# Performance work log

Measured on AMD Instinct MI355X. Metric: run time of the kernel, lower is better.

## Reference

```python
import jax, jax.numpy as jnp
import numpy as np

PAD_IDX = 0  # y_vocab.token_to_idx('<PAD>'); source also hard-codes argmax==0 as stop
B, N, M, V, T = 8, 6, 64, 32000, 8  # N = max_span, T = template_len


def setup_inputs() -> dict:
    key = jax.random.key(0)
    k1, k2, k3 = jax.random.split(key, 3)
    input_decodings = jax.random.normal(k1, (B, N, M, V), dtype=jnp.float32)
    template = jax.random.uniform(k2, (B, T, N + 1), dtype=jnp.float32)
    spans = jax.random.randint(k3, (B,), 0, N)
    return {"input_decodings": input_decodings, "template": template, "spans": spans}


def reference(input_decodings, template, spans):
    Bq, Nq, Mq, Vq = input_decodings.shape
    Tq = template.shape[1]
    # original only reads template[i, t, :spans[i]+1]; zero out the rest
    span_mask = jnp.arange(Nq + 1)[None, None, :] <= spans[:, None, None]
    tmpl = jnp.where(span_mask, template, jnp.zeros((), template.dtype))
    # choices[b] = [pad_vector, flatten(input_decodings[b,0]), ..., flatten(input_decodings[b,N-1])]
    pad_vec = jnp.zeros((Mq * Vq,), input_decodings.dtype).at[PAD_IDX].set(1.0)
    choices = jnp.concatenate(
        [jnp.broadcast_to(pad_vec, (Bq, 1, Mq * Vq)), input_decodings.reshape(Bq, Nq, Mq * Vq)],
        axis=1,
    )  # [B, N+1, M*V]
    # all per-step template matmuls at once: [B, T, M, V]
    outputs = jnp.einsum('bts,bsd->btd', tmpl, choices).reshape(Bq, Tq, Mq, Vq)

    pos = jnp.arange(Mq)

    def step(carry, out_t):
        idx, result = carry  # idx: [B] int, result: [B, M, V]
        amax = jnp.argmax(out_t, axis=-1)  # [B, M]
        iszero = amax == 0
        # length of leading run of nonzero argmax (stop at first zero)
        out_len = jnp.where(jnp.any(iszero, axis=1), jnp.argmax(iszero, axis=1).astype(jnp.int32), Mq)
        out_len = jnp.minimum(out_len, Mq - idx)
        wmask = (pos[None, :] >= idx[:, None]) & (pos[None, :] < (idx + out_len)[:, None])  # [B, M]
        gather_idx = jnp.clip(pos[None, :] - idx[:, None], 0, Mq - 1)  # [B, M]
        src = jnp.take_along_axis(out_t, gather_idx[:, :, None], axis=1)  # [B, M, V]
        result = jnp.where(wmask[:, :, None], src, result)
        return (idx + out_len, result), None

    init = (jnp.zeros((Bq,), jnp.int32), jnp.zeros((Bq, Mq, Vq), input_decodings.dtype))
    (final_idx, result), _ = jax.lax.scan(step, init, jnp.swapaxes(outputs, 0, 1))
    return result
```

## Files before the change

### kernel.cpp

```cpp
#include <hip/hip_runtime.h>
#include <math.h>

namespace {
constexpr int kB = 8;
constexpr int kN = 6;
constexpr int kM = 64;
constexpr int kV = 32000;
constexpr int kT = 8;
constexpr int kS = kN + 1;
constexpr int kV4 = kV / 4;
constexpr int kThreads = 256;
}

typedef float f32x4 __attribute__((ext_vector_type(4)));


template <int NUSE>
__device__ __forceinline__ void pass1_body(const float* __restrict__ in,
                                           const float* __restrict__ tw,
                                           float* __restrict__ orow,
                                           int b, int m,
                                           int* __restrict__ flags) {
  const int tid = threadIdx.x;
  constexpr int NA = NUSE > 0 ? NUSE : 1;

  float w[kT][NA];
  float w0[kT];
#pragma unroll
  for (int t = 0; t < kT; ++t) {
    w0[t] = tw[t * kS];
#pragma unroll
    for (int n = 0; n < NUSE; ++n) w[t][n] = tw[t * kS + n + 1];
  }

  const f32x4* rows[NA];
#pragma unroll
  for (int n = 0; n < NUSE; ++n)
    rows[n] = (const f32x4*)(in + ((size_t)(b * kN + n) * kM + m) * kV);

  f32x4* orow4 = (f32x4*)orow;

  float mx[kT], v0[kT];
#pragma unroll
  for (int t = 0; t < kT; ++t) {
    mx[t] = -INFINITY;
    v0[t] = 0.0f;
  }

  for (int v4 = tid; v4 < kV4; v4 += kThreads) {
    f32x4 x[NA];
#pragma unroll
    for (int n = 0; n < NUSE; ++n) x[n] = __builtin_nontemporal_load(&rows[n][v4]);
    const bool head = (v4 == 0);
#pragma unroll
    for (int t = 0; t < kT; ++t) {
      float ax = 0.0f, ay = 0.0f, az = 0.0f, aw = 0.0f;
#pragma unroll
      for (int n = 0; n < NUSE; ++n) {
        ax = fmaf(w[t][n], x[n].x, ax);
        ay = fmaf(w[t][n], x[n].y, ay);
        az = fmaf(w[t][n], x[n].z, az);
        aw = fmaf(w[t][n], x[n].w, aw);
      }
      if (head && m == 0) ax += w0[t];
      if (head) v0[t] = ax;
      mx[t] = fmaxf(mx[t], fmaxf(fmaxf(ax, ay), fmaxf(az, aw)));
      if (t == 0) {
        f32x4 o = {ax, ay, az, aw};
        __builtin_nontemporal_store(o, &orow4[v4]);
      }
    }
  }

  __shared__ float red[kT][4];
  const int lane = tid & 63;
  const int wv = tid >> 6;
#pragma unroll
  for (int t = 0; t < kT; ++t) {
    float v = mx[t];
#pragma unroll
    for (int off = 32; off > 0; off >>= 1) v = fmaxf(v, __shfl_xor(v, off, 64));
    if (lane == 0) red[t][wv] = v;
  }
  __syncthreads();
  if (tid == 0) {
#pragma unroll
    for (int t = 0; t < kT; ++t) {
      float bm = fmaxf(fmaxf(red[t][0], red[t][1]), fmaxf(red[t][2], red[t][3]));
      flags[(b * kT + t) * kM + m] = (v0[t] >= bm) ? 1 : 0;
    }
  }
}

__global__ __launch_bounds__(kThreads) void pass1_kernel(
    const float* __restrict__ in, const float* __restrict__ tmpl,
    const int* __restrict__ spans, float* __restrict__ out,
    int* __restrict__ flags) {
  const int blk = blockIdx.x;
  const int b = blk >> 6;
  const int m = blk & 63;
  int span = spans[b];
  int nuse = span < 0 ? 0 : (span > kN ? kN : span);
  const float* tw = tmpl + (size_t)b * kT * kS;
  float* orow = out + (size_t)(b * kM + m) * kV;
  switch (nuse) {
    case 0: pass1_body<0>(in, tw, orow, b, m, flags); break;
    case 1: pass1_body<1>(in, tw, orow, b, m, flags); break;
    case 2: pass1_body<2>(in, tw, orow, b, m, flags); break;
    case 3: pass1_body<3>(in, tw, orow, b, m, flags); break;
    case 4: pass1_body<4>(in, tw, orow, b, m, flags); break;
    case 5: pass1_body<5>(in, tw, orow, b, m, flags); break;
    case 6: pass1_body<6>(in, tw, orow, b, m, flags); break;
  }
}

__global__ __launch_bounds__(kThreads) void patch_kernel(
    const float* __restrict__ in, const float* __restrict__ tmpl,
    const int* __restrict__ spans, const int* __restrict__ flags,
    float* __restrict__ out) {
  const int blk = blockIdx.x;
  const int b = blk >> 6;
  const int m = blk & 63;
  const int tid = threadIdx.x;
  const int lane = tid & 63;

  __shared__ int slen[kT];
  if (tid < 64) {
#pragma unroll
    for (int t = 0; t < kT; ++t) {
      int f = flags[(b * kT + t) * kM + lane];
      unsigned long long bal = __ballot(f != 0);
      if (lane == 0) slen[t] = bal ? (int)(__ffsll((long long)bal) - 1) : kM;
    }
  }
  __syncthreads();

  int sel_t = -1, sel_row = 0, idx = 0;
#pragma unroll
  for (int t = 0; t < kT; ++t) {
    int L = slen[t];
    if (L > kM - idx) L = kM - idx;
    if (sel_t < 0 && m >= idx && m < idx + L) {
      sel_t = t;
      sel_row = m - idx;
    }
    idx += L;
  }

  if (sel_t == 0) return;

  float* orow = out + (size_t)(b * kM + m) * kV;
  f32x4* orow4 = (f32x4*)orow;

  if (sel_t < 0) {
    f32x4 z = {0.0f, 0.0f, 0.0f, 0.0f};
    for (int v4 = tid; v4 < kV4; v4 += kThreads)
      __builtin_nontemporal_store(z, &orow4[v4]);
    return;
  }

  const int t = sel_t;
  const int row = sel_row;
  int span = spans[b];
  int nuse = span < 0 ? 0 : (span > kN ? kN : span);
  const float* tw = tmpl + ((size_t)b * kT + t) * kS;
  const float w0 = tw[0];
  float w[kN];
  for (int n = 0; n < kN; ++n) w[n] = (n < nuse) ? tw[n + 1] : 0.0f;

  const f32x4* rows[kN];
  for (int n = 0; n < kN; ++n)
    rows[n] = (const f32x4*)(in + ((size_t)(b * kN + n) * kM + row) * kV);

  for (int v4 = tid; v4 < kV4; v4 += kThreads) {
    float ax = 0.0f, ay = 0.0f, az = 0.0f, aw = 0.0f;
    for (int n = 0; n < nuse; ++n) {
      f32x4 x = __builtin_nontemporal_load(&rows[n][v4]);
      ax = fmaf(w[n], x.x, ax);
      ay = fmaf(w[n], x.y, ay);
      az = fmaf(w[n], x.z, az);
      aw = fmaf(w[n], x.w, aw);
    }
    if (v4 == 0 && row == 0) ax += w0;
    f32x4 o = {ax, ay, az, aw};
    __builtin_nontemporal_store(o, &orow4[v4]);
  }
}

extern "C" void kernel_launch(void* const* d_in, const int* in_sizes, int n_in,
                              void* d_out, int out_size, void* d_ws,
                              size_t ws_size, hipStream_t stream) {
  const float* in = (const float*)d_in[0];
  const float* tmpl = (const float*)d_in[1];
  const int* spans = (const int*)d_in[2];
  float* out = (float*)d_out;

  int* flags = (int*)d_ws;

  hipLaunchKernelGGL(pass1_kernel, dim3(kB * kM), dim3(kThreads), 0, stream,
                     in, tmpl, spans, out, flags);
  hipLaunchKernelGGL(patch_kernel, dim3(kB * kM), dim3(kThreads), 0, stream,
                     in, tmpl, spans, flags, out);
}
```

Measured before the change: 485.5 us.

## Split pass1 vocab scan across four blocks per row with partial max reduction

```diff
diff --git a/kernel.cpp b/kernel.cpp
--- a/kernel.cpp
+++ b/kernel.cpp
@@ -8,7 +8,9 @@
 constexpr int kV = 32000;
 constexpr int kT = 8;
 constexpr int kS = kN + 1;
+constexpr int kC = 4;
 constexpr int kV4 = kV / 4;
+constexpr int kCV4 = kV4 / kC;
 constexpr int kThreads = 256;
 }
 
@@ -19,8 +21,9 @@
 __device__ __forceinline__ void pass1_body(const float* __restrict__ in,
                                            const float* __restrict__ tw,
                                            float* __restrict__ orow,
-                                           int b, int m,
-                                           int* __restrict__ flags) {
+                                           int b, int m, int c,
+                                           float* __restrict__ pmax,
+                                           float* __restrict__ v0g) {
   const int tid = threadIdx.x;
   constexpr int NA = NUSE > 0 ? NUSE : 1;
 
@@ -36,7 +39,8 @@
   const f32x4* rows[NA];
 #pragma unroll
   for (int n = 0; n < NUSE; ++n)
-    rows[n] = (const f32x4*)(in + ((size_t)(b * kN + n) * kM + m) * kV);
+    rows[n] = (const f32x4*)(in + ((size_t)(b * kN + n) * kM + m) * kV) +
+              (size_t)c * kCV4;
 
   f32x4* orow4 = (f32x4*)orow;
 
@@ -47,11 +51,12 @@
     v0[t] = 0.0f;
   }
 
-  for (int v4 = tid; v4 < kV4; v4 += kThreads) {
+  const bool headblk = (c == 0);
+  for (int v4 = tid; v4 < kCV4; v4 += kThreads) {
     f32x4 x[NA];
 #pragma unroll
     for (int n = 0; n < NUSE; ++n) x[n] = __builtin_nontemporal_load(&rows[n][v4]);
-    const bool head = (v4 == 0);
+    const bool head = headblk && (v4 == 0);
 #pragma unroll
     for (int t = 0; t < kT; ++t) {
       float ax = 0.0f, ay = 0.0f, az = 0.0f, aw = 0.0f;
@@ -87,7 +92,8 @@
 #pragma unroll
     for (int t = 0; t < kT; ++t) {
       float bm = fmaxf(fmaxf(red[t][0], red[t][1]), fmaxf(red[t][2], red[t][3]));
-      flags[(b * kT + t) * kM + m] = (v0[t] >= bm) ? 1 : 0;
+      pmax[((b * kT + t) * kM + m) * kC + c] = bm;
+      if (headblk) v0g[(b * kT + t) * kM + m] = v0[t];
     }
   }
 }
@@ -95,29 +101,30 @@
 __global__ __launch_bounds__(kThreads) void pass1_kernel(
     const float* __restrict__ in, const float* __restrict__ tmpl,
     const int* __restrict__ spans, float* __restrict__ out,
-    int* __restrict__ flags) {
+    float* __restrict__ pmax, float* __restrict__ v0g) {
   const int blk = blockIdx.x;
-  const int b = blk >> 6;
-  const int m = blk & 63;
+  const int c = blk & (kC - 1);
+  const int m = (blk >> 2) & 63;
+  const int b = blk >> 8;
   int span = spans[b];
   int nuse = span < 0 ? 0 : (span > kN ? kN : span);
   const float* tw = tmpl + (size_t)b * kT * kS;
-  float* orow = out + (size_t)(b * kM + m) * kV;
+  float* orow = out + (size_t)(b * kM + m) * kV + (size_t)c * kCV4 * 4;
   switch (nuse) {
-    case 0: pass1_body<0>(in, tw, orow, b, m, flags); break;
-    case 1: pass1_body<1>(in, tw, orow, b, m, flags); break;
-    case 2: pass1_body<2>(in, tw, orow, b, m, flags); break;
-    case 3: pass1_body<3>(in, tw, orow, b, m, flags); break;
-    case 4: pass1_body<4>(in, tw, orow, b, m, flags); break;
-    case 5: pass1_body<5>(in, tw, orow, b, m, flags); break;
-    case 6: pass1_body<6>(in, tw, orow, b, m, flags); break;
+    case 0: pass1_body<0>(in, tw, orow, b, m, c, pmax, v0g); break;
+    case 1: pass1_body<1>(in, tw, orow, b, m, c, pmax, v0g); break;
+    case 2: pass1_body<2>(in, tw, orow, b, m, c, pmax, v0g); break;
+    case 3: pass1_body<3>(in, tw, orow, b, m, c, pmax, v0g); break;
+    case 4: pass1_body<4>(in, tw, orow, b, m, c, pmax, v0g); break;
+    case 5: pass1_body<5>(in, tw, orow, b, m, c, pmax, v0g); break;
+    case 6: pass1_body<6>(in, tw, orow, b, m, c, pmax, v0g); break;
   }
 }
 
 __global__ __launch_bounds__(kThreads) void patch_kernel(
     const float* __restrict__ in, const float* __restrict__ tmpl,
-    const int* __restrict__ spans, const int* __restrict__ flags,
-    float* __restrict__ out) {
+    const int* __restrict__ spans, const float* __restrict__ pmax,
+    const float* __restrict__ v0g, float* __restrict__ out) {
   const int blk = blockIdx.x;
   const int b = blk >> 6;
   const int m = blk & 63;
@@ -128,8 +135,10 @@
   if (tid < 64) {
 #pragma unroll
     for (int t = 0; t < kT; ++t) {
-      int f = flags[(b * kT + t) * kM + lane];
-      unsigned long long bal = __ballot(f != 0);
+      f32x4 p = *(const f32x4*)&pmax[((b * kT + t) * kM + lane) * kC];
+      float bm = fmaxf(fmaxf(p.x, p.y), fmaxf(p.z, p.w));
+      float v0 = v0g[(b * kT + t) * kM + lane];
+      unsigned long long bal = __ballot(v0 >= bm);
       if (lane == 0) slen[t] = bal ? (int)(__ffsll((long long)bal) - 1) : kM;
     }
   }
@@ -195,10 +204,11 @@
   const int* spans = (const int*)d_in[2];
   float* out = (float*)d_out;
 
-  int* flags = (int*)d_ws;
-
-  hipLaunchKernelGGL(pass1_kernel, dim3(kB * kM), dim3(kThreads), 0, stream,
-                     in, tmpl, spans, out, flags);
+  float* pmax = (float*)d_ws;
+  float* v0g = pmax + kB * kT * kM * kC;
+
+  hipLaunchKernelGGL(pass1_kernel, dim3(kB * kM * kC), dim3(kThreads), 0,
+                     stream, in, tmpl, spans, out, pmax, v0g);
   hipLaunchKernelGGL(patch_kernel, dim3(kB * kM), dim3(kThreads), 0, stream,
-                     in, tmpl, spans, flags, out);
-}
+                     in, tmpl, spans, pmax, v0g, out);
+}
```

New measurement: 485.7 us. No clear change (+0.0%).
